# Kernel tuning notes

Measured on AMD Instinct MI355X. Metric: run time of the kernel, lower is better.

Reference implementation:

```python
import jax, jax.numpy as jnp
import numpy as np

EPS = 1e-5
K = 5          # kernel size from SE3Convolution(5, ...)
STRIDE = 2
PAD = 3
C_HID = 52     # 4*dim(repr3x3=9) + dim(repr7=7) + dim(repr9=9)
N_CLASSES = 10


def conv3d(x, w):
    # x: [N, Cin, D, H, W], w: [Cout, Cin, K, K, K]
    return jax.lax.conv_general_dilated(
        x, w,
        window_strides=(STRIDE, STRIDE, STRIDE),
        padding=[(PAD, PAD)] * 3,
        dimension_numbers=("NCDHW", "OIDHW", "NCDHW"),
    )


def bn3d(x):
    # training-mode batch norm over (batch, spatial), per channel, no affine
    mean = jnp.mean(x, axis=(0, 2, 3, 4), keepdims=True)
    var = jnp.var(x, axis=(0, 2, 3, 4), keepdims=True)
    return (x - mean) * jax.lax.rsqrt(var + EPS)


def setup_inputs() -> dict:
    key = jax.random.key(0)
    ks = jax.random.split(key, 10)
    x = jax.random.normal(ks[0], (32, 1, 64, 64, 64), dtype=jnp.float32)
    s = 0.05
    w0 = jax.random.normal(ks[1], (C_HID, 1, K, K, K), jnp.float32) * s
    b0 = jax.random.normal(ks[2], (C_HID,), jnp.float32) * s
    w1 = jax.random.normal(ks[3], (C_HID, C_HID, K, K, K), jnp.float32) * s
    b1 = jax.random.normal(ks[4], (C_HID,), jnp.float32) * s
    w2 = jax.random.normal(ks[5], (C_HID, C_HID, K, K, K), jnp.float32) * s
    b2 = jax.random.normal(ks[6], (C_HID,), jnp.float32) * s
    w3 = jax.random.normal(ks[7], (N_CLASSES, C_HID, K, K, K), jnp.float32) * s
    gamma = jnp.ones((N_CLASSES,), jnp.float32)
    beta = jnp.zeros((N_CLASSES,), jnp.float32)
    return {"x": x, "w0": w0, "b0": b0, "w1": w1, "b1": b1,
            "w2": w2, "b2": b2, "w3": w3, "gamma": gamma, "beta": beta}


def reference(x, w0, b0, w1, b1, w2, b2, w3, gamma, beta):
    # bn_in: BatchNorm3d(1, affine=False)
    h = bn3d(x)
    # three conv blocks with scalar batch norm + bias + ReLU (non_lin layers)
    for w, b in ((w0, b0), (w1, b1), (w2, b2)):
        h = conv3d(h, w)
        h = bn3d(h)
        h = jax.nn.relu(h + b[None, :, None, None, None])
    # final conv (no nonlinearity)
    h = conv3d(h, w3)
    # global average pool over x, y, z -> [batch, classes]
    h = jnp.mean(h, axis=(2, 3, 4))
    # bn_out: affine batch norm over the batch dim, per class
    mean = jnp.mean(h, axis=0, keepdims=True)
    var = jnp.var(h, axis=0, keepdims=True)
    h = (h - mean) * jax.lax.rsqrt(var + EPS)
    return h * gamma[None, :] + beta[None, :]
```

## Files before the change

### kernel.cpp

```cpp
#include <hip/hip_runtime.h>
#include <hip/hip_bf16.h>

#define EPSV 1e-5f
constexpr int NB = 32;

typedef short bf16x8 __attribute__((ext_vector_type(8)));
typedef short short4v __attribute__((ext_vector_type(4)));
typedef float f32x4 __attribute__((ext_vector_type(4)));

__device__ inline float bf2f(short s) {
  return __uint_as_float(((unsigned)(unsigned short)s) << 16);
}
__device__ inline short f2bf(float f) {
  unsigned u = __float_as_uint(f);
  unsigned r = (u + 0x7FFFu + ((u >> 16) & 1u)) >> 16;
  return (short)r;
}

__global__ __launch_bounds__(256) void reduce_partial_f32(
    const float* __restrict__ in, int spatial, float* __restrict__ part,
    int totb, int boff)
{
  const int b = blockIdx.x;
  const int nblk = gridDim.x;
  float s = 0.f, s2 = 0.f;
  for (int n = 0; n < NB; ++n) {
    const float* p = in + (size_t)n * spatial;
    for (int i = b * 256 + threadIdx.x; i < spatial; i += nblk * 256) {
      float v = p[i];
      s += v; s2 += v * v;
    }
  }
  __shared__ float sh[256], sh2[256];
  int tid = threadIdx.x;
  sh[tid] = s; sh2[tid] = s2;
  __syncthreads();
  for (int off = 128; off > 0; off >>= 1) {
    if (tid < off) { sh[tid] += sh[tid + off]; sh2[tid] += sh2[tid + off]; }
    __syncthreads();
  }
  if (tid == 0) {
    part[(size_t)(boff + b) * 2 + 0] = sh[0];
    part[(size_t)(boff + b) * 2 + 1] = sh2[0];
  }
}

__global__ __launch_bounds__(256) void reduce_cl(
    const short* __restrict__ y, long nrows,
    float* __restrict__ part, int totb, int boff)
{
  const int b = blockIdx.x, nblk = gridDim.x;
  const int c = threadIdx.x & 63, seg = threadIdx.x >> 6;
  float s = 0.f, s2 = 0.f;
  for (long r = (long)b * 4 + seg; r < nrows; r += (long)nblk * 4) {
    float v = bf2f(y[r * 64 + c]);
    s += v; s2 += v * v;
  }
  __shared__ float sh[4][64], sh2[4][64];
  sh[seg][c] = s; sh2[seg][c] = s2;
  __syncthreads();
  if (seg == 0) {
    float a = sh[0][c] + sh[1][c] + sh[2][c] + sh[3][c];
    float a2 = sh2[0][c] + sh2[1][c] + sh2[2][c] + sh2[3][c];
    part[((size_t)c * totb + boff + b) * 2 + 0] = a;
    part[((size_t)c * totb + boff + b) * 2 + 1] = a2;
  }
}

__global__ __launch_bounds__(64) void reduce_final(
    const float* __restrict__ part, int nblk, int C, float* __restrict__ sums)
{
  const int c = blockIdx.x;
  float s = 0.f, s2 = 0.f;
  for (int b = threadIdx.x; b < nblk; b += 64) {
    s  += part[((size_t)c * nblk + b) * 2 + 0];
    s2 += part[((size_t)c * nblk + b) * 2 + 1];
  }
  for (int off = 32; off > 0; off >>= 1) {
    s  += __shfl_down(s, off);
    s2 += __shfl_down(s2, off);
  }
  if (threadIdx.x == 0) { sums[c] = s; sums[C + c] = s2; }
}

__global__ __launch_bounds__(64) void aff_k(
    const float* __restrict__ st, const float* __restrict__ bias,
    float cnt_inv, int creal, float* __restrict__ a, float* __restrict__ c)
{
  int t = threadIdx.x;
  float mean = st[t] * cnt_inv;
  float var  = st[64 + t] * cnt_inv - mean * mean;
  float inv  = rsqrtf(var + EPSV);
  bool ok = t < creal;
  a[t] = ok ? inv : 0.f;
  c[t] = ok ? (-mean * inv + bias[t]) : 0.f;
}

__global__ __launch_bounds__(256) void repack_k(
    const float* __restrict__ w, short* __restrict__ wt,
    int CO, int CIN, int COP)
{
  long total = 125L * COP * 64;
  for (long idx = (long)blockIdx.x * 256 + threadIdx.x; idx < total;
       idx += (long)gridDim.x * 256) {
    int tap = (int)(idx / (COP * 64));
    int r   = (int)(idx % (COP * 64));
    int co = r >> 6, ci = r & 63;
    float v = (co < CO && ci < CIN) ? w[((size_t)co * CIN + ci) * 125 + tap] : 0.f;
    wt[idx] = f2bf(v);
  }
}

__global__ __launch_bounds__(256) void repack_w0(
    const float* __restrict__ w, short* __restrict__ wt)
{
  for (int idx = blockIdx.x * 256 + threadIdx.x; idx < 64 * 128;
       idx += gridDim.x * 256) {
    int co = idx >> 7, k = idx & 127;
    float v = (co < 52 && k < 125) ? w[co * 125 + k] : 0.f;
    wt[idx] = f2bf(v);
  }
}

__global__ __launch_bounds__(256) void conv0_mfma(
    const float* __restrict__ x, const short* __restrict__ w0t,
    const float* __restrict__ stats, short* __restrict__ out,
    int n_in0, int n_out0)
{
  constexpr int IN = 64, OUT = 33;
  constexpr float CNTI = 1.0f / ((float)NB * IN * IN * IN);
  __shared__ __align__(16) char slab[64 * 256];

  const int tid = threadIdx.x;
  const int wv = tid >> 6, ln = tid & 63;
  const int cs = ln >> 4;
  const int ntile0 = blockIdx.x * 64;
  const int od = blockIdx.y;
  const int img = blockIdx.z;

  const float mean = stats[0] * CNTI;
  const float inv  = rsqrtf(stats[1] * CNTI - mean * mean + EPSV);

  bf16x8 afr[4];
  {
    const short* wrow = w0t + (wv * 16 + (ln & 15)) * 128 + cs * 8;
    #pragma unroll
    for (int ks = 0; ks < 4; ++ks) afr[ks] = *(const bf16x8*)(wrow + ks * 32);
  }

  const float* xi = x + (size_t)(n_in0 + img) * (IN * IN * IN);
  const int id_base = 2 * od - 3;
  for (int u = tid; u < 1024; u += 256) {
    const int nl = u >> 4, s = u & 15;
    const int ng = ntile0 + nl;
    const int oh = ng / OUT, ow = ng - oh * OUT;
    const bool nok = ng < OUT * OUT;
    const int ih_base = 2 * oh - 3, iw_base = 2 * ow - 3;
    bf16x8 pk;
    #pragma unroll
    for (int e = 0; e < 8; ++e) {
      const int k = s * 8 + e;
      float f = 0.f;
      if (nok && k < 125) {
        const int kd = k / 25, r = k - kd * 25;
        const int kh = r / 5, kw = r - kh * 5;
        const int id = id_base + kd, ih = ih_base + kh, iw = iw_base + kw;
        if ((unsigned)id < (unsigned)IN && (unsigned)ih < (unsigned)IN &&
            (unsigned)iw < (unsigned)IN)
          f = (xi[((size_t)id * IN + ih) * IN + iw] - mean) * inv;
      }
      pk[e] = f2bf(f);
    }
    const int slot = (s & 8) | ((s & 7) ^ (nl & 7));
    *(bf16x8*)(slab + nl * 256 + slot * 16) = pk;
  }
  __syncthreads();

  const int nl = ln & 15;
  #pragma unroll
  for (int nt = 0; nt < 4; ++nt) {
    f32x4 acc = (f32x4){0.f, 0.f, 0.f, 0.f};
    const int nn = nt * 16 + nl;
    #pragma unroll
    for (int ks = 0; ks < 4; ++ks) {
      const int s = ks * 4 + cs;
      const int slot = (s & 8) | ((s & 7) ^ (nn & 7));
      bf16x8 b = *(const bf16x8*)(slab + nn * 256 + slot * 16);
      acc = __builtin_amdgcn_mfma_f32_16x16x32_bf16(afr[ks], b, acc, 0, 0, 0);
    }
    const int ng = ntile0 + nn;
    if (ng < OUT * OUT) {
      const int oh = ng / OUT, ow = ng - oh * OUT;
      short4v pk;
      #pragma unroll
      for (int r = 0; r < 4; ++r) pk[r] = f2bf(acc[r]);
      size_t base = ((((size_t)(n_out0 + img) * OUT + od) * OUT + oh) * OUT + ow) * 64;
      *(short4v*)(out + base + wv * 16 + cs * 4) = pk;
    }
  }
}

__device__ inline int swz(int lin, int cs) {
  int row = lin >> 1;
  int slot = (((lin & 1) << 2) | cs) ^ (row & 7);
  return row * 128 + slot * 16;
}

__device__ __forceinline__ void loada2(bf16x8 (&dst)[2][5], const short* __restrict__ wt,
                                       int tapb, int ch, int wm, int nl, int cs) {
  #pragma unroll
  for (int mi = 0; mi < 2; ++mi)
    #pragma unroll
    for (int kw = 0; kw < 5; ++kw)
      dst[mi][kw] = *(const bf16x8*)(
          wt + ((size_t)(tapb + kw) * 64 + (2 * wm + mi) * 16 + nl) * 64 + ch * 32 + cs * 8);
}

template<int IN, int OUT, int OHG>
__global__ __launch_bounds__(256, 2) void conv_2m2n(
    const short* __restrict__ yin, const short* __restrict__ wt,
    const float* __restrict__ affa, const float* __restrict__ affc,
    short* __restrict__ yout, int n_in0, int n_out0)
{
  constexpr int W = 2 * OUT + 3;
  constexpr int H = 2 * OHG + 3;
  constexpr int LIN = H * W;
  constexpr int ROWS = (LIN + 1) / 2;
  constexpr int LINM = LIN - 1 - 4 * W - 4;

  __shared__ __align__(16) char slab[ROWS * 128];
  __shared__ float s_a[64], s_c[64];

  const int tid = threadIdx.x;
  const int wv = tid >> 6, ln = tid & 63;
  const int nl = ln & 15, cs = ln >> 4;
  const int wm = wv >> 1, wn = wv & 1;
  const int oh0 = blockIdx.x * OHG;
  const int od  = blockIdx.y;
  const int nimg = blockIdx.z;

  if (tid < 64) { s_a[tid] = affa[tid]; s_c[tid] = affc[tid]; }

  int lb[2]; bool vld[2]; size_t obase[2];
  #pragma unroll
  for (int j = 0; j < 2; ++j) {
    int nt = 2 * wn + j;
    int n = nt * 16 + nl;
    int ohl = n / OUT, ow = n - ohl * OUT;
    vld[j] = n < OHG * OUT;
    int l = 2 * ohl * W + 2 * ow;
    lb[j] = (l > LINM) ? LINM : l;
    obase[j] = ((((size_t)(n_out0 + nimg) * OUT + od) * OUT + (oh0 + ohl)) * OUT + ow) * 64;
  }

  f32x4 acc[2][2];
  #pragma unroll
  for (int mi = 0; mi < 2; ++mi)
    #pragma unroll
    for (int j = 0; j < 2; ++j) acc[mi][j] = (f32x4){0.f, 0.f, 0.f, 0.f};

  const int id_base = 2 * od - 3;
  const int ih_base = 2 * oh0 - 3;

  for (int ch = 0; ch < 2; ++ch) {
    for (int kd = 0; kd < 5; ++kd) {
      __syncthreads();
      {
        const int id = id_base + kd;
        const bool dok = (unsigned)id < (unsigned)IN;
        for (int u = tid; u < LIN * 4; u += 256) {
          int lin = u >> 2, cs2 = u & 3;
          int hl = lin / W, wl = lin - hl * W;
          int ih = ih_base + hl;
          int iw = wl - 3;
          bf16x8 pk;
          if (dok && (unsigned)ih < (unsigned)IN && (unsigned)iw < (unsigned)IN) {
            size_t base = ((((size_t)nimg * IN + id) * IN + ih) * IN + iw) * 64
                          + ch * 32 + cs2 * 8;
            bf16x8 ld = *(const bf16x8*)(yin + base);
            #pragma unroll
            for (int e = 0; e < 8; ++e) {
              int c = ch * 32 + cs2 * 8 + e;
              pk[e] = f2bf(fmaxf(s_a[c] * bf2f(ld[e]) + s_c[c], 0.f));
            }
          } else {
            #pragma unroll
            for (int e = 0; e < 8; ++e) pk[e] = 0;
          }
          *(bf16x8*)(slab + swz(lin, cs2)) = pk;
        }
      }
      bf16x8 afr[2][2][5];
      loada2(afr[0], wt, (kd * 5 + 0) * 5, ch, wm, nl, cs);
      __builtin_amdgcn_sched_barrier(0);
      __syncthreads();
      #pragma unroll
      for (int kh = 0; kh < 5; ++kh) {
        if (kh < 4)
          loada2(afr[(kh + 1) & 1], wt, (kd * 5 + kh + 1) * 5, ch, wm, nl, cs);
        __builtin_amdgcn_sched_barrier(0);
        #pragma unroll
        for (int kw = 0; kw < 5; ++kw) {
          bf16x8 b0 = *(const bf16x8*)(slab + swz(lb[0] + kh * W + kw, cs));
          bf16x8 b1 = *(const bf16x8*)(slab + swz(lb[1] + kh * W + kw, cs));
          #pragma unroll
          for (int mi = 0; mi < 2; ++mi) {
            acc[mi][0] = __builtin_amdgcn_mfma_f32_16x16x32_bf16(
                afr[kh & 1][mi][kw], b0, acc[mi][0], 0, 0, 0);
            acc[mi][1] = __builtin_amdgcn_mfma_f32_16x16x32_bf16(
                afr[kh & 1][mi][kw], b1, acc[mi][1], 0, 0, 0);
          }
        }
      }
    }
  }

  #pragma unroll
  for (int j = 0; j < 2; ++j) {
    if (!vld[j]) continue;
    #pragma unroll
    for (int mi = 0; mi < 2; ++mi) {
      short4v pk;
      #pragma unroll
      for (int r = 0; r < 4; ++r) pk[r] = f2bf(acc[mi][j][r]);
      *(short4v*)(yout + obase[j] + (2 * wm + mi) * 16 + cs * 4) = pk;
    }
  }
}

__global__ __launch_bounds__(256) void conv3_m(
    const short* __restrict__ yin, const short* __restrict__ wt,
    const float* __restrict__ affa, const float* __restrict__ affc,
    short* __restrict__ yout)
{
  constexpr int IN = 10, OUT = 6;
  constexpr int W = 15, H = 15, LIN = 225, ROWS = 113;
  constexpr int LINM = LIN - 1 - 4 * W - 4;
  __shared__ __align__(16) char slab[ROWS * 128];
  __shared__ float s_a[64], s_c[64];

  const int tid = threadIdx.x, wv = tid >> 6, ln = tid & 63;
  const int nl = ln & 15, cs = ln >> 4;
  const int od = blockIdx.x, nimg = blockIdx.y;

  if (tid < 64) { s_a[tid] = affa[tid]; s_c[tid] = affc[tid]; }

  const int nn = wv * 16 + nl;
  const bool act = wv < 3;
  const bool vld = act && nn < 36;
  int ohl = nn / 6, ow = nn - ohl * 6;
  int lb = 2 * ohl * W + 2 * ow;
  if (lb > LINM) lb = LINM;
  const size_t obase = ((((size_t)nimg * 6 + od) * 6 + ohl) * 6 + ow) * 16;

  f32x4 acc = (f32x4){0.f, 0.f, 0.f, 0.f};
  const int id_base = 2 * od - 3;

  for (int ch = 0; ch < 2; ++ch) {
    for (int kd = 0; kd < 5; ++kd) {
      const int id = id_base + kd;
      const bool dok = (unsigned)id < (unsigned)IN;
      __syncthreads();
      for (int u = tid; u < 900; u += 256) {
        int lin = u >> 2, cs2 = u & 3;
        int hl = lin / 15, wl = lin - hl * 15;
        int ih = hl - 3, iw = wl - 3;
        bf16x8 pk;
        if (dok && (unsigned)ih < (unsigned)IN && (unsigned)iw < (unsigned)IN) {
          bf16x8 ld = *(const bf16x8*)(yin + ((((size_t)nimg * IN + id) * IN + ih) * IN + iw) * 64
                                       + ch * 32 + cs2 * 8);
          #pragma unroll
          for (int e = 0; e < 8; ++e) {
            int c = ch * 32 + cs2 * 8 + e;
            pk[e] = f2bf(fmaxf(s_a[c] * bf2f(ld[e]) + s_c[c], 0.f));
          }
        } else {
          #pragma unroll
          for (int e = 0; e < 8; ++e) pk[e] = 0;
        }
        *(bf16x8*)(slab + swz(lin, cs2)) = pk;
      }
      __syncthreads();
      if (act) {
        for (int kh = 0; kh < 5; ++kh) {
          const int tapb = (kd * 5 + kh) * 5;
          bf16x8 afr[5];
          #pragma unroll
          for (int kw = 0; kw < 5; ++kw)
            afr[kw] = *(const bf16x8*)(wt + ((size_t)(tapb + kw) * 16 + nl) * 64
                                       + ch * 32 + cs * 8);
          #pragma unroll
          for (int kw = 0; kw < 5; ++kw) {
            bf16x8 b = *(const bf16x8*)(slab + swz(lb + kh * W + kw, cs));
            acc = __builtin_amdgcn_mfma_f32_16x16x32_bf16(afr[kw], b, acc, 0, 0, 0);
          }
        }
      }
    }
  }
  if (vld) {
    short4v pk;
    #pragma unroll
    for (int r = 0; r < 4; ++r) pk[r] = f2bf(acc[r]);
    *(short4v*)(yout + obase + cs * 4) = pk;
  }
}

__global__ __launch_bounds__(320) void pool_bn(
    const short* __restrict__ y3, const float* __restrict__ gamma,
    const float* __restrict__ beta, float* __restrict__ out)
{
  __shared__ float pool[320];
  const int t = threadIdx.x;
  const int n = t / 10, c = t % 10;
  const short* p = y3 + (size_t)n * 216 * 16 + c;
  float s = 0.f;
  for (int i = 0; i < 216; ++i) s += bf2f(p[i * 16]);
  const float pv = s * (1.0f / 216.0f);
  pool[t] = pv;
  __syncthreads();
  float m = 0.f, m2 = 0.f;
  for (int nn = 0; nn < 32; ++nn) {
    float v = pool[nn * 10 + c];
    m += v; m2 += v * v;
  }
  m *= (1.0f / 32.0f);
  m2 = m2 * (1.0f / 32.0f) - m * m;
  out[t] = (pv - m) * rsqrtf(m2 + EPSV) * gamma[c] + beta[c];
}

extern "C" void kernel_launch(void* const* d_in, const int* in_sizes, int n_in,
                              void* d_out, int out_size, void* d_ws, size_t ws_size,
                              hipStream_t stream)
{
  const float* x  = (const float*)d_in[0];
  const float* w0 = (const float*)d_in[1];
  const float* b0 = (const float*)d_in[2];
  const float* w1 = (const float*)d_in[3];
  const float* b1 = (const float*)d_in[4];
  const float* w2 = (const float*)d_in[5];
  const float* b2 = (const float*)d_in[6];
  const float* w3 = (const float*)d_in[7];
  const float* gamma = (const float*)d_in[8];
  const float* beta  = (const float*)d_in[9];
  float* out = (float*)d_out;

  char* base = (char*)d_ws;
  size_t off = 0;
  auto alloc = [&](size_t bytes) -> void* {
    void* p = base + off;
    off = (off + bytes + 255) & ~(size_t)255;
    return p;
  };
  short* y1  = (short*)alloc((size_t)32 * 5832 * 64 * 2);
  short* y2  = (short*)alloc((size_t)32 * 1000 * 64 * 2);
  short* y3  = (short*)alloc((size_t)32 * 216 * 16 * 2);
  short* w1t = (short*)alloc((size_t)125 * 64 * 64 * 2);
  short* w2t = (short*)alloc((size_t)125 * 64 * 64 * 2);
  short* w3t = (short*)alloc((size_t)125 * 16 * 64 * 2);
  short* w0t = (short*)alloc((size_t)64 * 128 * 2);
  float* st_in = (float*)alloc(1024);
  float* st0 = (float*)alloc(1024);
  float* st1 = (float*)alloc(1024);
  float* st2 = (float*)alloc(1024);
  float* a0 = (float*)alloc(256); float* c0 = (float*)alloc(256);
  float* a1 = (float*)alloc(256); float* c1 = (float*)alloc(256);
  float* a2 = (float*)alloc(256); float* c2 = (float*)alloc(256);
  float* part = (float*)alloc(64 * 1024 * 2 * 4);
  short* y0 = (short*)(base + off);
  size_t rem = (ws_size > off + 256) ? (ws_size - off - 256) : 0;
  const size_t Y0_IMG = (size_t)35937 * 64;
  int CH;
  if      (rem >= Y0_IMG * 32 * 2) CH = 32;
  else if (rem >= Y0_IMG * 16 * 2) CH = 16;
  else if (rem >= Y0_IMG * 8 * 2)  CH = 8;
  else if (rem >= Y0_IMG * 4 * 2)  CH = 4;
  else if (rem >= Y0_IMG * 2 * 2)  CH = 2;
  else                             CH = 1;
  const int nch = 32 / CH;

  repack_k<<<512, 256, 0, stream>>>(w1, w1t, 52, 52, 64);
  repack_k<<<512, 256, 0, stream>>>(w2, w2t, 52, 52, 64);
  repack_k<<<256, 256, 0, stream>>>(w3, w3t, 10, 52, 16);
  repack_w0<<<32, 256, 0, stream>>>(w0, w0t);

  reduce_partial_f32<<<128, 256, 0, stream>>>(x, 64 * 64 * 64, part, 128, 0);
  reduce_final<<<1, 64, 0, stream>>>(part, 128, 1, st_in);

  const float cnt0 = 1.0f / ((float)NB * 35937.0f);
  const float cnt1 = 1.0f / ((float)NB * 5832.0f);
  const float cnt2 = 1.0f / ((float)NB * 1000.0f);

  if (CH == 32) {
    conv0_mfma<<<dim3(18, 33, 32), 256, 0, stream>>>(x, w0t, st_in, y0, 0, 0);
    reduce_cl<<<1024, 256, 0, stream>>>(y0, (long)32 * 35937, part, 1024, 0);
    reduce_final<<<64, 64, 0, stream>>>(part, 1024, 64, st0);
    aff_k<<<1, 64, 0, stream>>>(st0, b0, cnt0, 52, a0, c0);
    conv_2m2n<33, 18, 3><<<dim3(6, 18, 32), 256, 0, stream>>>(
        y0, w1t, a0, c0, y1, 0, 0);
  } else {
    for (int ck = 0; ck < nch; ++ck) {
      conv0_mfma<<<dim3(18, 33, CH), 256, 0, stream>>>(x, w0t, st_in, y0, ck * CH, 0);
      reduce_cl<<<32, 256, 0, stream>>>(y0, (long)CH * 35937, part, nch * 32, ck * 32);
    }
    reduce_final<<<64, 64, 0, stream>>>(part, nch * 32, 64, st0);
    aff_k<<<1, 64, 0, stream>>>(st0, b0, cnt0, 52, a0, c0);
    for (int ck = 0; ck < nch; ++ck) {
      conv0_mfma<<<dim3(18, 33, CH), 256, 0, stream>>>(x, w0t, st_in, y0, ck * CH, 0);
      conv_2m2n<33, 18, 3><<<dim3(6, 18, CH), 256, 0, stream>>>(
          y0, w1t, a0, c0, y1, 0, ck * CH);
    }
  }

  reduce_cl<<<256, 256, 0, stream>>>(y1, (long)32 * 5832, part, 256, 0);
  reduce_final<<<64, 64, 0, stream>>>(part, 256, 64, st1);
  aff_k<<<1, 64, 0, stream>>>(st1, b1, cnt1, 52, a1, c1);

  conv_2m2n<18, 10, 5><<<dim3(2, 10, 32), 256, 0, stream>>>(
      y1, w2t, a1, c1, y2, 0, 0);

  reduce_cl<<<32, 256, 0, stream>>>(y2, (long)32 * 1000, part, 32, 0);
  reduce_final<<<64, 64, 0, stream>>>(part, 32, 64, st2);
  aff_k<<<1, 64, 0, stream>>>(st2, b2, cnt2, 52, a2, c2);

  conv3_m<<<dim3(6, 32), 256, 0, stream>>>(y2, w3t, a2, c2, y3);

  pool_bn<<<1, 320, 0, stream>>>(y3, gamma, beta, out);
}
```

Measured before the change: 1.618 ms.

## Stage all 64 channels per depth slice in LDS and remap blocks across XCDs

The conv kernel now loads the full 64-channel input slab for each kd into LDS once, instead of looping over two 32-channel halves, each of which reloads the spatial halo. This halves the number of slab fills and the __syncthreads barriers. It also switches to a 1D grid whose block index is remapped so that consecutive tiles land on the same XCD, which should improve L2 locality. The trade-off is double the LDS footprint per block, which may limit occupancy at 2 blocks per CU for the larger layer.

```diff
diff --git a/kernel.cpp b/kernel.cpp
--- a/kernel.cpp
+++ b/kernel.cpp
@@ -200,12 +200,6 @@
   }
 }
 
-__device__ inline int swz(int lin, int cs) {
-  int row = lin >> 1;
-  int slot = (((lin & 1) << 2) | cs) ^ (row & 7);
-  return row * 128 + slot * 16;
-}
-
 __device__ __forceinline__ void loada2(bf16x8 (&dst)[2][5], const short* __restrict__ wt,
                                        int tapb, int ch, int wm, int nl, int cs) {
   #pragma unroll
@@ -217,27 +211,36 @@
 }
 
 template<int IN, int OUT, int OHG>
-__global__ __launch_bounds__(256, 2) void conv_2m2n(
+__global__ __launch_bounds__(256, 2) void conv_full(
     const short* __restrict__ yin, const short* __restrict__ wt,
     const float* __restrict__ affa, const float* __restrict__ affc,
-    short* __restrict__ yout, int n_in0, int n_out0)
+    short* __restrict__ yout, int n_out0)
 {
   constexpr int W = 2 * OUT + 3;
   constexpr int H = 2 * OHG + 3;
   constexpr int LIN = H * W;
-  constexpr int ROWS = (LIN + 1) / 2;
+  constexpr int OHT = (OUT + OHG - 1) / OHG;
   constexpr int LINM = LIN - 1 - 4 * W - 4;
 
-  __shared__ __align__(16) char slab[ROWS * 128];
+  __shared__ __align__(16) char slab[LIN * 128];
   __shared__ float s_a[64], s_c[64];
 
   const int tid = threadIdx.x;
   const int wv = tid >> 6, ln = tid & 63;
   const int nl = ln & 15, cs = ln >> 4;
   const int wm = wv >> 1, wn = wv & 1;
-  const int oh0 = blockIdx.x * OHG;
-  const int od  = blockIdx.y;
-  const int nimg = blockIdx.z;
+
+  int lin;
+  if (gridDim.x & 7) lin = blockIdx.x;
+  else {
+    const int q = gridDim.x >> 3;
+    lin = (blockIdx.x & 7) * q + (blockIdx.x >> 3);
+  }
+  const int oht = lin % OHT;
+  const int t2  = lin / OHT;
+  const int od  = t2 % OUT;
+  const int img = t2 / OUT;
+  const int oh0 = oht * OHG;
 
   if (tid < 64) { s_a[tid] = affa[tid]; s_c[tid] = affc[tid]; }
 
@@ -250,7 +253,7 @@
     vld[j] = n < OHG * OUT;
     int l = 2 * ohl * W + 2 * ow;
     lb[j] = (l > LINM) ? LINM : l;
-    obase[j] = ((((size_t)(n_out0 + nimg) * OUT + od) * OUT + (oh0 + ohl)) * OUT + ow) * 64;
+    obase[j] = ((((size_t)(n_out0 + img) * OUT + od) * OUT + (oh0 + ohl)) * OUT + ow) * 64;
   }
 
   f32x4 acc[2][2];
@@ -262,47 +265,53 @@
   const int id_base = 2 * od - 3;
   const int ih_base = 2 * oh0 - 3;
 
-  for (int ch = 0; ch < 2; ++ch) {
-    for (int kd = 0; kd < 5; ++kd) {
-      __syncthreads();
-      {
-        const int id = id_base + kd;
-        const bool dok = (unsigned)id < (unsigned)IN;
-        for (int u = tid; u < LIN * 4; u += 256) {
-          int lin = u >> 2, cs2 = u & 3;
-          int hl = lin / W, wl = lin - hl * W;
-          int ih = ih_base + hl;
-          int iw = wl - 3;
-          bf16x8 pk;
-          if (dok && (unsigned)ih < (unsigned)IN && (unsigned)iw < (unsigned)IN) {
-            size_t base = ((((size_t)nimg * IN + id) * IN + ih) * IN + iw) * 64
-                          + ch * 32 + cs2 * 8;
-            bf16x8 ld = *(const bf16x8*)(yin + base);
-            #pragma unroll
-            for (int e = 0; e < 8; ++e) {
-              int c = ch * 32 + cs2 * 8 + e;
-              pk[e] = f2bf(fmaxf(s_a[c] * bf2f(ld[e]) + s_c[c], 0.f));
-            }
-          } else {
-            #pragma unroll
-            for (int e = 0; e < 8; ++e) pk[e] = 0;
+  for (int kd = 0; kd < 5; ++kd) {
+    __syncthreads();
+    {
+      const int id = id_base + kd;
+      const bool dok = (unsigned)id < (unsigned)IN;
+      for (int u = tid; u < LIN * 8; u += 256) {
+        int v = u >> 3, cc = u & 7;
+        int hl = v / W, wl = v - hl * W;
+        int ih = ih_base + hl;
+        int iw = wl - 3;
+        bf16x8 pk;
+        if (dok && (unsigned)ih < (unsigned)IN && (unsigned)iw < (unsigned)IN) {
+          size_t base = ((((size_t)img * IN + id) * IN + ih) * IN + iw) * 64 + cc * 8;
+          bf16x8 ld = *(const bf16x8*)(yin + base);
+          #pragma unroll
+          for (int e = 0; e < 8; ++e) {
+            int c = cc * 8 + e;
+            pk[e] = f2bf(fmaxf(s_a[c] * bf2f(ld[e]) + s_c[c], 0.f));
           }
-          *(bf16x8*)(slab + swz(lin, cs2)) = pk;
+        } else {
+          #pragma unroll
+          for (int e = 0; e < 8; ++e) pk[e] = 0;
         }
+        *(bf16x8*)(slab + v * 128 + ((cc ^ ((v >> 1) & 7)) << 4)) = pk;
       }
-      bf16x8 afr[2][2][5];
-      loada2(afr[0], wt, (kd * 5 + 0) * 5, ch, wm, nl, cs);
-      __builtin_amdgcn_sched_barrier(0);
-      __syncthreads();
+    }
+    bf16x8 afr[2][2][5];
+    loada2(afr[0], wt, kd * 25, 0, wm, nl, cs);
+    __builtin_amdgcn_sched_barrier(0);
+    __syncthreads();
+    for (int ch = 0; ch < 2; ++ch) {
+      if (ch == 1) {
+        loada2(afr[0], wt, kd * 25, 1, wm, nl, cs);
+        __builtin_amdgcn_sched_barrier(0);
+      }
       #pragma unroll
       for (int kh = 0; kh < 5; ++kh) {
         if (kh < 4)
-          loada2(afr[(kh + 1) & 1], wt, (kd * 5 + kh + 1) * 5, ch, wm, nl, cs);
+          loada2(afr[(kh + 1) & 1], wt, kd * 25 + (kh + 1) * 5, ch, wm, nl, cs);
         __builtin_amdgcn_sched_barrier(0);
         #pragma unroll
         for (int kw = 0; kw < 5; ++kw) {
-          bf16x8 b0 = *(const bf16x8*)(slab + swz(lb[0] + kh * W + kw, cs));
-          bf16x8 b1 = *(const bf16x8*)(slab + swz(lb[1] + kh * W + kw, cs));
+          const int v0 = lb[0] + kh * W + kw;
+          const int v1 = lb[1] + kh * W + kw;
+          const int cc = ch * 4 + cs;
+          bf16x8 b0 = *(const bf16x8*)(slab + v0 * 128 + ((cc ^ ((v0 >> 1) & 7)) << 4));
+          bf16x8 b1 = *(const bf16x8*)(slab + v1 * 128 + ((cc ^ ((v1 >> 1) & 7)) << 4));
           #pragma unroll
           for (int mi = 0; mi < 2; ++mi) {
             acc[mi][0] = __builtin_amdgcn_mfma_f32_16x16x32_bf16(
@@ -328,13 +337,19 @@
   }
 }
 
+__device__ inline int swz(int lin, int cs) {
+  int row = lin >> 1;
+  int slot = (((lin & 1) << 2) | cs) ^ (row & 7);
+  return row * 128 + slot * 16;
+}
+
 __global__ __launch_bounds__(256) void conv3_m(
     const short* __restrict__ yin, const short* __restrict__ wt,
     const float* __restrict__ affa, const float* __restrict__ affc,
     short* __restrict__ yout)
 {
   constexpr int IN = 10, OUT = 6;
-  constexpr int W = 15, H = 15, LIN = 225, ROWS = 113;
+  constexpr int W = 15, LIN = 225, ROWS = 113;
   constexpr int LINM = LIN - 1 - 4 * W - 4;
   __shared__ __align__(16) char slab[ROWS * 128];
   __shared__ float s_a[64], s_c[64];
@@ -496,8 +511,8 @@
     reduce_cl<<<1024, 256, 0, stream>>>(y0, (long)32 * 35937, part, 1024, 0);
     reduce_final<<<64, 64, 0, stream>>>(part, 1024, 64, st0);
     aff_k<<<1, 64, 0, stream>>>(st0, b0, cnt0, 52, a0, c0);
-    conv_2m2n<33, 18, 3><<<dim3(6, 18, 32), 256, 0, stream>>>(
-        y0, w1t, a0, c0, y1, 0, 0);
+    conv_full<33, 18, 3><<<6 * 18 * 32, 256, 0, stream>>>(
+        y0, w1t, a0, c0, y1, 0);
   } else {
     for (int ck = 0; ck < nch; ++ck) {
       conv0_mfma<<<dim3(18, 33, CH), 256, 0, stream>>>(x, w0t, st_in, y0, ck * CH, 0);
@@ -507,8 +522,8 @@
     aff_k<<<1, 64, 0, stream>>>(st0, b0, cnt0, 52, a0, c0);
     for (int ck = 0; ck < nch; ++ck) {
       conv0_mfma<<<dim3(18, 33, CH), 256, 0, stream>>>(x, w0t, st_in, y0, ck * CH, 0);
-      conv_2m2n<33, 18, 3><<<dim3(6, 18, CH), 256, 0, stream>>>(
-          y0, w1t, a0, c0, y1, 0, ck * CH);
+      conv_full<33, 18, 3><<<6 * 18 * CH, 256, 0, stream>>>(
+          y0, w1t, a0, c0, y1, ck * CH);
     }
   }
 
@@ -516,8 +531,8 @@
   reduce_final<<<64, 64, 0, stream>>>(part, 256, 64, st1);
   aff_k<<<1, 64, 0, stream>>>(st1, b1, cnt1, 52, a1, c1);
 
-  conv_2m2n<18, 10, 5><<<dim3(2, 10, 32), 256, 0, stream>>>(
-      y1, w2t, a1, c1, y2, 0, 0);
+  conv_full<18, 10, 5><<<2 * 10 * 32, 256, 0, stream>>>(
+      y1, w2t, a1, c1, y2, 0);
 
   reduce_cl<<<32, 256, 0, stream>>>(y2, (long)32 * 1000, part, 32, 0);
   reduce_final<<<64, 64, 0, stream>>>(part, 32, 64, st2);
```

New measurement: 1.595 ms. About the same (-1.4%).
